# Performance work log

Measured on AMD Instinct MI355X. Metric: run time of the kernel, lower is better.

The kernel has to match this reference:

```python
import jax, jax.numpy as jnp
import numpy as np

N, E, ED, ENH, H, T_STEPS = 2000, 64000, 16, 128, 64, 8


def setup_inputs() -> dict:
    key = jax.random.key(0)
    ks = jax.random.split(key, 8)
    s = 0.05
    return {
        "x": jax.random.normal(ks[0], (N, H), jnp.float32),
        "adj": jnp.zeros((N, N), jnp.float32),
        "edge_data": jax.random.normal(ks[1], (N, N, ED), jnp.float32),
        "edges": jax.random.randint(ks[2], (E, 2), 0, N),
        "T": T_STEPS,
        "W1": jax.random.normal(ks[3], (ED, ENH), jnp.float32) * s,
        "b1": jnp.zeros((ENH,), jnp.float32),
        "W2": jax.random.normal(ks[4], (ENH, H * H), jnp.float32) * s,
        "b2": jnp.zeros((H * H,), jnp.float32),
        "W_ih": jax.random.normal(ks[5], (2 * H, 3 * H), jnp.float32) * s,
        "W_hh": jax.random.normal(ks[6], (H, 3 * H), jnp.float32) * s,
        "b_ih": jnp.zeros((3 * H,), jnp.float32),
        "b_hh": jnp.zeros((3 * H,), jnp.float32),
    }


def _gru_cell(inp, h, W_ih, W_hh, b_ih, b_hh):
    # PyTorch GRUCell, gates ordered (r, z, n); weights stored transposed.
    gi = inp @ W_ih + b_ih
    gh = h @ W_hh + b_hh
    i_r, i_z, i_n = jnp.split(gi, 3, axis=-1)
    h_r, h_z, h_n = jnp.split(gh, 3, axis=-1)
    r = jax.nn.sigmoid(i_r + h_r)
    z = jax.nn.sigmoid(i_z + h_z)
    n = jnp.tanh(i_n + r * h_n)
    return (1.0 - z) * n + z * h


def reference(x, adj, edge_data, edges, T, W1, b1, W2, b2, W_ih, W_hh, b_ih, b_hh):
    h_d = x.shape[1]
    src, tgt = edges[:, 0], edges[:, 1]
    # edge net: per-edge h_d x h_d matrix from dense edge_data[src, tgt]
    ef = edge_data[src, tgt]                                  # [E, e_d]
    h1 = jax.nn.relu(ef @ W1 + b1)                            # [E, en_d]
    A = jax.nn.relu(h1 @ W2 + b2).reshape(-1, h_d, h_d)       # [E, h, h]
    # original scatters the message A_e @ x[src_e] into BOTH endpoints
    # (edges[e,:].eq(v).any()); when src==tgt it is added only once.
    not_self = (src != tgt)[:, None]
    for _ in range(T):
        msg = jnp.einsum('eij,ej->ei', A, x[src])             # [E, h]
        m = jnp.zeros_like(x).at[tgt].add(msg)
        m = m.at[src].add(jnp.where(not_self, msg, 0.0))
        x = _gru_cell(jnp.concatenate([x, m], axis=1), x, W_ih, W_hh, b_ih, b_hh)
    return x
```

## Files before the change

### kernel.cpp

```cpp
#include <hip/hip_runtime.h>
#include <stdint.h>

#define N_NODES 2000
#define N_EDGES 64000
#define EDIM 16
#define ENH 128
#define HD 64
#define T_STEPS 8
#define HH 4096

typedef unsigned short u16;
typedef __bf16 bf16x8 __attribute__((ext_vector_type(8)));
typedef float float4v __attribute__((ext_vector_type(4)));
typedef unsigned int uint4v __attribute__((ext_vector_type(4)));

__device__ u16   g_h1_hi[(size_t)N_EDGES * ENH];
__device__ u16   g_h1_lo[(size_t)N_EDGES * ENH];
__device__ u16   g_w2t_hi[HH * ENH];
__device__ u16   g_w2t_lo[HH * ENH];
__device__ float g_scale[(N_EDGES / 16) * 32];

__device__ __forceinline__ float b2f(u16 h) {
    union { unsigned int u; float f; } v; v.u = ((unsigned int)h) << 16; return v.f;
}
__device__ __forceinline__ u16 f2b(float f) {
    union { float f; unsigned int u; } v; v.f = f;
    unsigned int u = v.u;
    return (u16)((u + 0x7FFFu + ((u >> 16) & 1u)) >> 16);
}

__global__ void k_xinit(const float* __restrict__ xin, float* __restrict__ x0,
                        float* __restrict__ m) {
    int i = blockIdx.x * 256 + threadIdx.x;
    if (i < N_NODES * HD) { x0[i] = xin[i]; m[i] = 0.f; }
}

__global__ __launch_bounds__(256) void k_h1(const float* __restrict__ edge_data,
                                            const int* __restrict__ edges,
                                            const float* __restrict__ W1,
                                            const float* __restrict__ b1) {
    int tid = threadIdx.x;
    int e = blockIdx.x * 2 + (tid >> 7);
    int c = tid & 127;
    int src = edges[2 * e], tgt = edges[2 * e + 1];
    const float* ef = edge_data + ((size_t)src * N_NODES + (size_t)tgt) * EDIM;
    float acc = b1[c];
#pragma unroll
    for (int k = 0; k < EDIM; k++)
        acc += ef[k] * W1[k * ENH + c];
    float v = fmaxf(acc, 0.f);
    u16 hi = f2b(v);
    size_t idx = (size_t)e * ENH + c;
    g_h1_hi[idx] = hi;
    g_h1_lo[idx] = f2b(v - b2f(hi));
}

__global__ void k_w2t(const float* __restrict__ W2) {
    int idx = blockIdx.x * 256 + threadIdx.x;
    int n = idx >> 7, k = idx & 127;
    float v = W2[(size_t)k * HH + n];
    u16 hi = f2b(v);
    g_w2t_hi[idx] = hi;
    g_w2t_lo[idx] = f2b(v - b2f(hi));
}

#define LDK 72
#define STK 136

__global__ __launch_bounds__(256, 2) void k_gemmA(const float* __restrict__ b2,
                                                  u16* __restrict__ Aq) {
    __shared__ __align__(16) u16 smem[4 * 128 * LDK];
    __shared__ float redmax[2][4][2];
    u16 (*sAh)[LDK] = (u16(*)[LDK])smem;
    u16 (*sAl)[LDK] = (u16(*)[LDK])(smem + 128 * LDK);
    u16 (*sBh)[LDK] = (u16(*)[LDK])(smem + 2 * 128 * LDK);
    u16 (*sBl)[LDK] = (u16(*)[LDK])(smem + 3 * 128 * LDK);
    u16 (*st)[STK]  = (u16(*)[STK])smem;

    int bid = (blockIdx.x & 7) * 2000 + (blockIdx.x >> 3);
    int cb = bid & 31;
    int rb = bid >> 5;
    int m0 = rb * 128, n0 = cb * 128;
    int t = threadIdx.x;
    int w = t >> 6, l = t & 63;
    int wm = w >> 1, wn = w & 1;
    int quad = l >> 4, lr = l & 15;

    float4v acc[4][4];
#pragma unroll
    for (int mi = 0; mi < 4; mi++)
#pragma unroll
        for (int ni = 0; ni < 4; ni++) acc[mi][ni] = (float4v){0.f, 0.f, 0.f, 0.f};

#pragma unroll
    for (int kc = 0; kc < 2; kc++) {
        if (kc) __syncthreads();
#pragma unroll
        for (int rnd = 0; rnd < 4; rnd++) {
            int c = rnd * 256 + t;
            int row = c >> 3, c8 = c & 7;
            size_t gA = ((size_t)(m0 + row) << 7) + (kc << 6) + (c8 << 3);
            size_t gB = ((size_t)(n0 + row) << 7) + (kc << 6) + (c8 << 3);
            *(uint4*)&sAh[row][c8 * 8] = *(const uint4*)(g_h1_hi + gA);
            *(uint4*)&sAl[row][c8 * 8] = *(const uint4*)(g_h1_lo + gA);
            *(uint4*)&sBh[row][c8 * 8] = *(const uint4*)(g_w2t_hi + gB);
            *(uint4*)&sBl[row][c8 * 8] = *(const uint4*)(g_w2t_lo + gB);
        }
        __syncthreads();
#pragma unroll
        for (int kq = 0; kq < 2; kq++) {
            int ko = kq * 32 + quad * 8;
            bf16x8 ah[4], al[4], bh[4], bl[4];
#pragma unroll
            for (int i = 0; i < 4; i++) {
                ah[i] = *(const bf16x8*)&sAh[wm * 64 + i * 16 + lr][ko];
                al[i] = *(const bf16x8*)&sAl[wm * 64 + i * 16 + lr][ko];
                bh[i] = *(const bf16x8*)&sBh[wn * 64 + i * 16 + lr][ko];
                bl[i] = *(const bf16x8*)&sBl[wn * 64 + i * 16 + lr][ko];
            }
#pragma unroll
            for (int mi = 0; mi < 4; mi++)
#pragma unroll
                for (int ni = 0; ni < 4; ni++) {
                    acc[mi][ni] = __builtin_amdgcn_mfma_f32_16x16x32_bf16(ah[mi], bh[ni], acc[mi][ni], 0, 0, 0);
                    acc[mi][ni] = __builtin_amdgcn_mfma_f32_16x16x32_bf16(ah[mi], bl[ni], acc[mi][ni], 0, 0, 0);
                    acc[mi][ni] = __builtin_amdgcn_mfma_f32_16x16x32_bf16(al[mi], bh[ni], acc[mi][ni], 0, 0, 0);
                }
        }
    }

    float wmax[4];
#pragma unroll
    for (int mi = 0; mi < 4; mi++) {
        float lm = 0.f;
#pragma unroll
        for (int ni = 0; ni < 4; ni++) {
            float bias = b2[n0 + wn * 64 + ni * 16 + lr];
#pragma unroll
            for (int r = 0; r < 4; r++) {
                float v = fmaxf(acc[mi][ni][r] + bias, 0.f);
                acc[mi][ni][r] = v;
                lm = fmaxf(lm, v);
            }
        }
#pragma unroll
        for (int ofs = 32; ofs > 0; ofs >>= 1)
            lm = fmaxf(lm, __shfl_xor(lm, ofs));
        wmax[mi] = lm;
    }
    if (l == 0) {
#pragma unroll
        for (int mi = 0; mi < 4; mi++) redmax[wm][mi][wn] = wmax[mi];
    }
    __syncthreads();

    float inv[4];
#pragma unroll
    for (int mi = 0; mi < 4; mi++) {
        float cm = fmaxf(redmax[wm][mi][0], redmax[wm][mi][1]);
        inv[mi] = (cm > 0.f) ? (65535.f / cm) : 0.f;
        if (wn == 0 && l == 0)
            g_scale[(size_t)((m0 + wm * 64 + mi * 16) >> 4) * 32 + cb] = cm * (1.f / 65535.f);
    }

#pragma unroll
    for (int mi = 0; mi < 4; mi++)
#pragma unroll
        for (int ni = 0; ni < 4; ni++) {
            int col = wn * 64 + ni * 16 + lr;
#pragma unroll
            for (int r = 0; r < 4; r++) {
                u16 q = (u16)fminf(acc[mi][ni][r] * inv[mi] + 0.5f, 65535.f);
                st[wm * 64 + mi * 16 + quad * 4 + r][col] = q;
            }
        }
    __syncthreads();

#pragma unroll
    for (int rnd = 0; rnd < 8; rnd++) {
        int c = rnd * 256 + t;
        int row = c >> 4, ch = c & 15;
        uint4 v = *(const uint4*)&st[row][ch * 8];
        *(uint4*)(Aq + (size_t)(m0 + row) * HH + n0 + ch * 8) = v;
    }
}

__global__ __launch_bounds__(256) void k_edge(const u16* __restrict__ Aq,
                                              const float* __restrict__ xcur,
                                              const int* __restrict__ edges,
                                              float* __restrict__ m) {
    int gid = blockIdx.x * 256 + threadIdx.x;
    int e = gid >> 6;
    int l = gid & 63;
    int src = edges[2 * e], tgt = edges[2 * e + 1];
    const float4* xp = (const float4*)(xcur + (size_t)src * HD + (l & 7) * 8);
    float4 xa = xp[0], xb = xp[1];
    const uint4v* ap = (const uint4v*)(Aq + (size_t)e * HH);
    uint4v a[8];
#pragma unroll
    for (int t = 0; t < 8; t++)
        a[t] = __builtin_nontemporal_load(&ap[t * 64 + l]);
    float msgv = 0.f;
#pragma unroll
    for (int t = 0; t < 8; t++) {
        float p;
        p  = (float)(a[t].x & 0xFFFFu) * xa.x + (float)(a[t].x >> 16) * xa.y;
        p += (float)(a[t].y & 0xFFFFu) * xa.z + (float)(a[t].y >> 16) * xa.w;
        p += (float)(a[t].z & 0xFFFFu) * xb.x + (float)(a[t].z >> 16) * xb.y;
        p += (float)(a[t].w & 0xFFFFu) * xb.z + (float)(a[t].w >> 16) * xb.w;
        p += __shfl_xor(p, 1);
        p += __shfl_xor(p, 2);
        p += __shfl_xor(p, 4);
        msgv = ((l & 7) == t) ? p : msgv;
    }
    int r = (l & 7) * 8 + (l >> 3);
    float scale = g_scale[(e >> 4) * 32 + (r >> 1)];
    float msg = msgv * scale;
    unsafeAtomicAdd(&m[(size_t)tgt * HD + r], msg);
    if (src != tgt) unsafeAtomicAdd(&m[(size_t)src * HD + r], msg);
}

__global__ __launch_bounds__(256) void k_gru(const float* __restrict__ xcur,
                                             float* __restrict__ m,
                                             const float* __restrict__ W_ih,
                                             const float* __restrict__ W_hh,
                                             const float* __restrict__ b_ih,
                                             const float* __restrict__ b_hh,
                                             float* __restrict__ xnext,
                                             float* __restrict__ out, int write_out) {
    int v = blockIdx.x;
    int tid = threadIdx.x;
    int j = tid & 63;
    int kq = tid >> 6;
    __shared__ float xs[HD], ms[HD];
    __shared__ float red[4][6][HD];
    if (tid < HD) {
        xs[tid] = xcur[v * HD + tid];
        ms[tid] = m[v * HD + tid];
    }
    __syncthreads();
    float gir = 0.f, giz = 0.f, gin = 0.f;
    float ghr = 0.f, ghz = 0.f, ghn = 0.f;
#pragma unroll
    for (int ki = 0; ki < 16; ki++) {
        int k = kq * 16 + ki;
        float xk = xs[k], mk = ms[k];
        const float* wi_x = W_ih + k * 192;
        const float* wi_m = W_ih + (64 + k) * 192;
        const float* wh = W_hh + k * 192;
        gir += xk * wi_x[j] + mk * wi_m[j];
        giz += xk * wi_x[64 + j] + mk * wi_m[64 + j];
        gin += xk * wi_x[128 + j] + mk * wi_m[128 + j];
        ghr += xk * wh[j];
        ghz += xk * wh[64 + j];
        ghn += xk * wh[128 + j];
    }
    red[kq][0][j] = gir; red[kq][1][j] = giz; red[kq][2][j] = gin;
    red[kq][3][j] = ghr; red[kq][4][j] = ghz; red[kq][5][j] = ghn;
    __syncthreads();
    if (kq == 0) {
        float sgir = b_ih[j]       + red[0][0][j] + red[1][0][j] + red[2][0][j] + red[3][0][j];
        float sgiz = b_ih[64 + j]  + red[0][1][j] + red[1][1][j] + red[2][1][j] + red[3][1][j];
        float sgin = b_ih[128 + j] + red[0][2][j] + red[1][2][j] + red[2][2][j] + red[3][2][j];
        float sghr = b_hh[j]       + red[0][3][j] + red[1][3][j] + red[2][3][j] + red[3][3][j];
        float sghz = b_hh[64 + j]  + red[0][4][j] + red[1][4][j] + red[2][4][j] + red[3][4][j];
        float sghn = b_hh[128 + j] + red[0][5][j] + red[1][5][j] + red[2][5][j] + red[3][5][j];
        float r = 1.f / (1.f + __expf(-(sgir + sghr)));
        float z = 1.f / (1.f + __expf(-(sgiz + sghz)));
        float n = tanhf(sgin + r * sghn);
        float xn = (1.f - z) * n + z * xs[j];
        xnext[v * HD + j] = xn;
        m[v * HD + j] = 0.f;
        if (write_out) out[v * HD + j] = xn;
    }
}

extern "C" void kernel_launch(void* const* d_in, const int* in_sizes, int n_in,
                              void* d_out, int out_size, void* d_ws, size_t ws_size,
                              hipStream_t stream) {
    (void)in_sizes; (void)n_in; (void)out_size; (void)ws_size;
    const float* x_in      = (const float*)d_in[0];
    const float* edge_data = (const float*)d_in[2];
    const int*   edges     = (const int*)d_in[3];
    const float* W1   = (const float*)d_in[5];
    const float* b1   = (const float*)d_in[6];
    const float* W2   = (const float*)d_in[7];
    const float* b2   = (const float*)d_in[8];
    const float* W_ih = (const float*)d_in[9];
    const float* W_hh = (const float*)d_in[10];
    const float* b_ih = (const float*)d_in[11];
    const float* b_hh = (const float*)d_in[12];
    float* out = (float*)d_out;

    char* ws = (char*)d_ws;
    u16* Aq = (u16*)ws;
    size_t off = (size_t)N_EDGES * HH * sizeof(u16);
    float* xb0 = (float*)(ws + off); off += (size_t)N_NODES * HD * sizeof(float);
    float* xb1 = (float*)(ws + off); off += (size_t)N_NODES * HD * sizeof(float);
    float* m   = (float*)(ws + off); off += (size_t)N_NODES * HD * sizeof(float);

    k_xinit<<<(N_NODES * HD + 255) / 256, 256, 0, stream>>>(x_in, xb0, m);
    k_h1<<<N_EDGES / 2, 256, 0, stream>>>(edge_data, edges, W1, b1);
    k_w2t<<<(HH * 128) / 256, 256, 0, stream>>>(W2);
    k_gemmA<<<(N_EDGES / 128) * (HH / 128), 256, 0, stream>>>(b2, Aq);

    float* bufs[2] = {xb0, xb1};
    for (int t = 0; t < T_STEPS; t++) {
        k_edge<<<(N_EDGES * 64) / 256, 256, 0, stream>>>(Aq, bufs[t & 1], edges, m);
        k_gru<<<N_NODES, 256, 0, stream>>>(bufs[t & 1], m, W_ih, W_hh, b_ih, b_hh,
                                           bufs[(t + 1) & 1], out,
                                           (t == T_STEPS - 1) ? 1 : 0);
    }
}
```

Measured before the change: 1.457 ms.

## Double-buffer GEMM staging with direct global-to-LDS loads and XOR swizzle

Replaces the register-routed global->shared copies in the edge-matrix GEMM with global_load_lds direct transfers into an XOR-swizzled unpadded layout. It double-buffers four K-slices of 32 so the next slice loads while MFMAs run on the current one. This is meant to hide global latency and cut VGPR traffic and LDS bank conflicts. The LDS footprint stays similar (64KB). It relies on correct vmcnt waits and barriers, and on the swizzle matching both the writes and the reads.

```diff
diff --git a/kernel.cpp b/kernel.cpp
--- a/kernel.cpp
+++ b/kernel.cpp
@@ -27,6 +27,13 @@
     union { float f; unsigned int u; } v; v.f = f;
     unsigned int u = v.u;
     return (u16)((u + 0x7FFFu + ((u >> 16) & 1u)) >> 16);
+}
+
+__device__ __forceinline__ void gld_lds16(const void* g, void* l) {
+    __builtin_amdgcn_global_load_lds(
+        (const __attribute__((address_space(1))) unsigned int*)(uintptr_t)g,
+        (__attribute__((address_space(3))) unsigned int*)(unsigned int)(uintptr_t)l,
+        16, 0, 0);
 }
 
 __global__ void k_xinit(const float* __restrict__ xin, float* __restrict__ x0,
@@ -64,18 +71,15 @@
     g_w2t_lo[idx] = f2b(v - b2f(hi));
 }
 
-#define LDK 72
+#define PLANE 4096
+#define BUFU16 16384
 #define STK 136
 
 __global__ __launch_bounds__(256, 2) void k_gemmA(const float* __restrict__ b2,
                                                   u16* __restrict__ Aq) {
-    __shared__ __align__(16) u16 smem[4 * 128 * LDK];
+    __shared__ __align__(16) u16 smem[2 * BUFU16];
     __shared__ float redmax[2][4][2];
-    u16 (*sAh)[LDK] = (u16(*)[LDK])smem;
-    u16 (*sAl)[LDK] = (u16(*)[LDK])(smem + 128 * LDK);
-    u16 (*sBh)[LDK] = (u16(*)[LDK])(smem + 2 * 128 * LDK);
-    u16 (*sBl)[LDK] = (u16(*)[LDK])(smem + 3 * 128 * LDK);
-    u16 (*st)[STK]  = (u16(*)[STK])smem;
+    u16 (*st)[STK] = (u16(*)[STK])smem;
 
     int bid = (blockIdx.x & 7) * 2000 + (blockIdx.x >> 3);
     int cb = bid & 31;
@@ -92,41 +96,58 @@
 #pragma unroll
         for (int ni = 0; ni < 4; ni++) acc[mi][ni] = (float4v){0.f, 0.f, 0.f, 0.f};
 
-#pragma unroll
-    for (int kc = 0; kc < 2; kc++) {
-        if (kc) __syncthreads();
-#pragma unroll
-        for (int rnd = 0; rnd < 4; rnd++) {
-            int c = rnd * 256 + t;
-            int row = c >> 3, c8 = c & 7;
-            size_t gA = ((size_t)(m0 + row) << 7) + (kc << 6) + (c8 << 3);
-            size_t gB = ((size_t)(n0 + row) << 7) + (kc << 6) + (c8 << 3);
-            *(uint4*)&sAh[row][c8 * 8] = *(const uint4*)(g_h1_hi + gA);
-            *(uint4*)&sAl[row][c8 * 8] = *(const uint4*)(g_h1_lo + gA);
-            *(uint4*)&sBh[row][c8 * 8] = *(const uint4*)(g_w2t_hi + gB);
-            *(uint4*)&sBl[row][c8 * 8] = *(const uint4*)(g_w2t_lo + gB);
+    int srow = l >> 2;
+    int sc   = l & 3;
+
+    const char* gplane[4] = {(const char*)g_h1_hi, (const char*)g_h1_lo,
+                             (const char*)g_w2t_hi, (const char*)g_w2t_lo};
+
+    auto STAGE = [&](int ks, int bufIdx) {
+#pragma unroll
+        for (int i = 0; i < 8; i++) {
+            int plane = i >> 1;
+            int r0 = w * 32 + (i & 1) * 16;
+            int row = r0 + srow;
+            int cs = sc ^ ((row >> 1) & 3);
+            int base = (plane < 2) ? m0 : n0;
+            size_t gofs = ((size_t)(base + row) << 8) + ((size_t)ks << 6) + ((size_t)cs << 4);
+            char* lbase = (char*)smem + ((size_t)bufIdx << 15) + ((size_t)plane << 13) + ((size_t)r0 << 6);
+            gld_lds16(gplane[plane] + gofs, lbase);
         }
-        __syncthreads();
-#pragma unroll
-        for (int kq = 0; kq < 2; kq++) {
-            int ko = kq * 32 + quad * 8;
-            bf16x8 ah[4], al[4], bh[4], bl[4];
-#pragma unroll
-            for (int i = 0; i < 4; i++) {
-                ah[i] = *(const bf16x8*)&sAh[wm * 64 + i * 16 + lr][ko];
-                al[i] = *(const bf16x8*)&sAl[wm * 64 + i * 16 + lr][ko];
-                bh[i] = *(const bf16x8*)&sBh[wn * 64 + i * 16 + lr][ko];
-                bl[i] = *(const bf16x8*)&sBl[wn * 64 + i * 16 + lr][ko];
+    };
+
+    STAGE(0, 0);
+    asm volatile("s_waitcnt vmcnt(0)" ::: "memory");
+    __builtin_amdgcn_s_barrier();
+
+#pragma unroll
+    for (int ks = 0; ks < 4; ks++) {
+        if (ks < 3) STAGE(ks + 1, (ks + 1) & 1);
+
+        const char* bb = (const char*)smem + ((size_t)(ks & 1) << 15);
+        int sz = (lr >> 1) & 3;
+        size_t cofs = (size_t)((quad ^ sz) << 4);
+        bf16x8 ah[4], al[4], bh[4], bl[4];
+#pragma unroll
+        for (int i = 0; i < 4; i++) {
+            size_t ra = (size_t)(wm * 64 + i * 16 + lr) << 6;
+            size_t rbb = (size_t)(wn * 64 + i * 16 + lr) << 6;
+            ah[i] = *(const bf16x8*)(bb + ra + cofs);
+            al[i] = *(const bf16x8*)(bb + 8192 + ra + cofs);
+            bh[i] = *(const bf16x8*)(bb + 16384 + rbb + cofs);
+            bl[i] = *(const bf16x8*)(bb + 24576 + rbb + cofs);
+        }
+#pragma unroll
+        for (int mi = 0; mi < 4; mi++)
+#pragma unroll
+            for (int ni = 0; ni < 4; ni++) {
+                acc[mi][ni] = __builtin_amdgcn_mfma_f32_16x16x32_bf16(ah[mi], bh[ni], acc[mi][ni], 0, 0, 0);
+                acc[mi][ni] = __builtin_amdgcn_mfma_f32_16x16x32_bf16(ah[mi], bl[ni], acc[mi][ni], 0, 0, 0);
+                acc[mi][ni] = __builtin_amdgcn_mfma_f32_16x16x32_bf16(al[mi], bh[ni], acc[mi][ni], 0, 0, 0);
             }
-#pragma unroll
-            for (int mi = 0; mi < 4; mi++)
-#pragma unroll
-                for (int ni = 0; ni < 4; ni++) {
-                    acc[mi][ni] = __builtin_amdgcn_mfma_f32_16x16x32_bf16(ah[mi], bh[ni], acc[mi][ni], 0, 0, 0);
-                    acc[mi][ni] = __builtin_amdgcn_mfma_f32_16x16x32_bf16(ah[mi], bl[ni], acc[mi][ni], 0, 0, 0);
-                    acc[mi][ni] = __builtin_amdgcn_mfma_f32_16x16x32_bf16(al[mi], bh[ni], acc[mi][ni], 0, 0, 0);
-                }
-        }
+
+        asm volatile("s_waitcnt vmcnt(0)" ::: "memory");
+        __builtin_amdgcn_s_barrier();
     }
 
     float wmax[4];
```

New measurement: 1.462 ms. Within noise of the previous version (+0.4%).
